# Kernel tuning notes

Hardware: AMD Instinct MI355X
Metric: run time of the kernel (lower is better)

The kernel has to match this reference:

```python
import jax, jax.numpy as jnp
import numpy as np

N = 1_000_000
H = 256
DIMS = [1, H, H, H, H]
N_LAYERS = 4  # 4 linear layers, sin activation after the first 3


def setup_inputs() -> dict:
    key = jax.random.key(0)
    ks = jax.random.split(key, 1 + 2 * N_LAYERS)
    d = {"x": jax.random.normal(ks[0], (N, 2), dtype=jnp.float32)}
    i = 1
    for pre in ("x", "t"):
        for l in range(N_LAYERS):
            lim = 1.0 / np.sqrt(DIMS[l])  # torch.nn.Linear default init range
            d[f"{pre}W{l}"] = jax.random.uniform(
                ks[i], (DIMS[l], DIMS[l + 1]), dtype=jnp.float32, minval=-lim, maxval=lim)
            d[f"{pre}b{l}"] = jnp.zeros((DIMS[l + 1],), dtype=jnp.float32)
            i += 1
    return d


def _mlp(h, params):
    # params: list of (W, b); sin activation after all but the last layer
    n = len(params)
    for idx, (W, b) in enumerate(params):
        h = h @ W + b
        if idx < n - 1:
            h = jnp.sin(h)
    return h


def reference(x, xW0, xb0, xW1, xb1, xW2, xb2, xW3, xb3,
              tW0, tb0, tW1, tb1, tW2, tb2, tW3, tb3):
    x_params = [(xW0, xb0), (xW1, xb1), (xW2, xb2), (xW3, xb3)]
    t_params = [(tW0, tb0), (tW1, tb1), (tW2, tb2), (tW3, tb3)]
    nx = _mlp(x[:, 0:1], x_params)  # [N, H]
    nt = _mlp(x[:, 1:2], t_params)  # [N, H]
    # diag(A @ B.T) == rowwise dot product; avoids the O(N^2) matmul
    even = jnp.sum(nx[:, 0::2] * nt[:, 0::2], axis=-1)  # [N]
    odd = jnp.sum(nx[:, 1::2] * nt[:, 1::2], axis=-1)   # [N]
    return jnp.stack([even, odd], axis=-1)  # [N, 2]
```

## Files before the change

### kernel.cpp

```cpp
#include <hip/hip_runtime.h>


typedef _Float16 f16x8 __attribute__((ext_vector_type(8)));
typedef _Float16 f16x4 __attribute__((ext_vector_type(4)));
typedef float f32x4 __attribute__((ext_vector_type(4)));

__device__ __forceinline__ int hswz(int m, int kbyte) {
    return m * 512 + ((((kbyte >> 4) ^ (m & 7)) & 31) << 4) + (kbyte & 15);
}

__device__ __forceinline__ void barrier_lds() {
    asm volatile("s_waitcnt lgkmcnt(0)" ::: "memory");
    __builtin_amdgcn_s_barrier();
}

__global__ void prepack(const float* __restrict__ xW1, const float* __restrict__ xW2,
                        const float* __restrict__ xW3, const float* __restrict__ tW1,
                        const float* __restrict__ tW2, const float* __restrict__ tW3,
                        _Float16* __restrict__ dst)
{
    int g = blockIdx.x * 256 + threadIdx.x;
    int L = g >> 16;
    int r = g & 65535;
    int j  = r & 7;
    int l  = (r >> 3) & 63;
    int ci = (r >> 9) & 1;
    int w  = (r >> 10) & 7;
    int gg = (r >> 13) & 7;
    const float* W;
    switch (L) {
        case 0: W = xW1; break;
        case 1: W = xW2; break;
        case 2: W = xW3; break;
        case 3: W = tW1; break;
        case 4: W = tW2; break;
        default: W = tW3; break;
    }
    int n = w * 32 + ci * 16 + (l & 15);
    int k = gg * 32 + ((l >> 4) & 3) * 8 + j;
    dst[g] = (_Float16)W[k * 256 + n];
}


__device__ __forceinline__ void layer0_scalar(
    float xv, const float* __restrict__ W0, const float* __restrict__ b0,
    _Float16* __restrict__ hb, int tid)
{
    int m = tid >> 2;
    int q = tid & 3;
#pragma unroll
    for (int g = 0; g < 8; ++g) {
        int n0 = g * 32 + q * 8;
        f16x8 hv;
#pragma unroll
        for (int e = 0; e < 8; ++e) {
            float z = fmaf(xv, W0[n0 + e], b0[n0 + e]);
            hv[e] = (_Float16)__sinf(z);
        }
        *(f16x8*)((char*)hb + hswz(m, n0 * 2)) = hv;
    }
}

template<int MODE>
__device__ __forceinline__ void gemm_phase(
    const _Float16* __restrict__ Wl,
    const _Float16* __restrict__ Wnext,
    const _Float16* __restrict__ rb,
    f32x4 acc[2][8], f16x8 afr[2][2],
    f32x4 wacc[2][8],
    const float* __restrict__ wbias,
    _Float16* __restrict__ wb_lds,
    float xv,
    const float* __restrict__ W0,
    const float* __restrict__ b0,
    int tid, int lane, int ln, int quad, int wave)
{
    f32x4 zero = {0.f, 0.f, 0.f, 0.f};
#pragma unroll
    for (int ci = 0; ci < 2; ++ci)
#pragma unroll
        for (int ri = 0; ri < 8; ++ri)
            acc[ci][ri] = zero;

    const _Float16* abase = Wl + wave * 1024 + lane * 8;

    f16x8 bfr[8];
#pragma unroll
    for (int ri = 0; ri < 8; ++ri)
        bfr[ri] = *(const f16x8*)((const char*)rb +
                                  hswz(16 * ri + ln, quad * 16));

#pragma unroll
    for (int g = 0; g < 8; ++g) {
        __builtin_amdgcn_s_setprio(1);
#pragma unroll
        for (int ci = 0; ci < 2; ++ci)
#pragma unroll
            for (int ri = 0; ri < 8; ++ri)
                acc[ci][ri] = __builtin_amdgcn_mfma_f32_16x16x32_f16(
                    afr[g & 1][ci], bfr[ri], acc[ci][ri], 0, 0, 0);
        __builtin_amdgcn_s_setprio(0);

        if (g < 7) {
#pragma unroll
            for (int ri = 0; ri < 8; ++ri)
                bfr[ri] = *(const f16x8*)((const char*)rb +
                              hswz(16 * ri + ln, (g + 1) * 64 + quad * 16));
        }
        if (g < 6) {
#pragma unroll
            for (int ci = 0; ci < 2; ++ci)
                afr[g & 1][ci] = *(const f16x8*)(abase + (g + 2) * 8192 + ci * 512);
        } else if (Wnext) {
#pragma unroll
            for (int ci = 0; ci < 2; ++ci)
                afr[g & 1][ci] = *(const f16x8*)(Wnext + (g - 6) * 8192 +
                                                 wave * 1024 + lane * 8 + ci * 512);
        }

        if (MODE == 1) {
#pragma unroll
            for (int jo = 0; jo < 2; ++jo) {
                const int s  = g * 2 + jo;
                const int cw = s >> 3, rw = s & 7;
                const int nb = wave * 32 + cw * 16 + quad * 4;
                f32x4 bv = *(const f32x4*)&wbias[nb];
                f16x4 hv;
                hv[0] = (_Float16)__sinf(wacc[cw][rw][0] + bv[0]);
                hv[1] = (_Float16)__sinf(wacc[cw][rw][1] + bv[1]);
                hv[2] = (_Float16)__sinf(wacc[cw][rw][2] + bv[2]);
                hv[3] = (_Float16)__sinf(wacc[cw][rw][3] + bv[3]);
                *(f16x4*)((char*)wb_lds + hswz(16 * rw + ln, nb * 2)) = hv;
            }
        } else if (MODE == 2) {
            const int m = tid >> 2, q = tid & 3;
            const int n0 = g * 32 + q * 8;
            f16x8 hv;
#pragma unroll
            for (int e = 0; e < 8; ++e) {
                float z = fmaf(xv, W0[n0 + e], b0[n0 + e]);
                hv[e] = (_Float16)__sinf(z);
            }
            *(f16x8*)((char*)wb_lds + hswz(m, n0 * 2)) = hv;
        }
    }
}

__global__ __launch_bounds__(512, 2)
void mlp_fused(const float* __restrict__ x,
               const float* __restrict__ xW0, const float* __restrict__ xb0,
               const float* __restrict__ xb1, const float* __restrict__ xb2,
               const float* __restrict__ xb3,
               const float* __restrict__ tW0, const float* __restrict__ tb0,
               const float* __restrict__ tb1, const float* __restrict__ tb2,
               const float* __restrict__ tb3,
               const _Float16* __restrict__ Wp,
               float* __restrict__ out, int N)
{
    __shared__ __align__(16) _Float16 hbuf[2][128 * 256];
    __shared__ __align__(16) float    params[10 * 256];

    const int tid = threadIdx.x;
    const int lane = tid & 63;
    const int wave = tid >> 6;
    const int ln = lane & 15;
    const int quad = lane >> 4;
    const int row0 = blockIdx.x * 128;

    {
        const float* psrc[10] = {xW0, xb0, tW0, tb0, xb1, xb2, xb3, tb1, tb2, tb3};
        int half = tid >> 8, e = tid & 255;
#pragma unroll
        for (int s = 0; s < 5; ++s)
            params[(half * 5 + s) * 256 + e] = psrc[half * 5 + s][e];
    }
    const int myrow = row0 + (tid >> 2);
    const float2 xv2 = (myrow < N) ? ((const float2*)x)[myrow]
                                   : make_float2(0.f, 0.f);

    f32x4 xacc[2][8], tacc[2][8];
    f16x8 afr[2][2];

#pragma unroll
    for (int s = 0; s < 2; ++s)
#pragma unroll
        for (int ci = 0; ci < 2; ++ci)
            afr[s][ci] = *(const f16x8*)(Wp + s * 8192 + wave * 1024 +
                                         lane * 8 + ci * 512);
    barrier_lds();

    layer0_scalar(xv2.x, &params[0], &params[256], hbuf[0], tid);
    barrier_lds();

    gemm_phase<2>(Wp + 0 * 65536, Wp + 3 * 65536, hbuf[0], xacc, afr,
                  nullptr, nullptr, hbuf[1],
                  xv2.y, &params[2 * 256], &params[3 * 256],
                  tid, lane, ln, quad, wave);
    barrier_lds();
    gemm_phase<1>(Wp + 3 * 65536, Wp + 1 * 65536, hbuf[1], tacc, afr,
                  xacc, &params[4 * 256], hbuf[0],
                  0.f, nullptr, nullptr, tid, lane, ln, quad, wave);
    barrier_lds();
    gemm_phase<1>(Wp + 1 * 65536, Wp + 4 * 65536, hbuf[0], xacc, afr,
                  tacc, &params[7 * 256], hbuf[1],
                  0.f, nullptr, nullptr, tid, lane, ln, quad, wave);
    barrier_lds();
    gemm_phase<1>(Wp + 4 * 65536, Wp + 2 * 65536, hbuf[1], tacc, afr,
                  xacc, &params[5 * 256], hbuf[0],
                  0.f, nullptr, nullptr, tid, lane, ln, quad, wave);
    barrier_lds();
    gemm_phase<1>(Wp + 2 * 65536, Wp + 5 * 65536, hbuf[0], xacc, afr,
                  tacc, &params[8 * 256], hbuf[1],
                  0.f, nullptr, nullptr, tid, lane, ln, quad, wave);
    barrier_lds();
    gemm_phase<0>(Wp + 5 * 65536, nullptr, hbuf[1], tacc, afr,
                  nullptr, nullptr, nullptr,
                  0.f, nullptr, nullptr, tid, lane, ln, quad, wave);

    const float* xb3l = &params[6 * 256];
    const float* tb3l = &params[9 * 256];
    float ev[8], od[8];
#pragma unroll
    for (int ri = 0; ri < 8; ++ri) { ev[ri] = 0.f; od[ri] = 0.f; }
#pragma unroll
    for (int ci = 0; ci < 2; ++ci) {
        int nb = wave * 32 + ci * 16 + quad * 4;
        f32x4 xb = *(const f32x4*)&xb3l[nb];
        f32x4 tb = *(const f32x4*)&tb3l[nb];
#pragma unroll
        for (int ri = 0; ri < 8; ++ri) {
            float a0 = xacc[ci][ri][0] + xb[0], c0 = tacc[ci][ri][0] + tb[0];
            float a1 = xacc[ci][ri][1] + xb[1], c1 = tacc[ci][ri][1] + tb[1];
            float a2 = xacc[ci][ri][2] + xb[2], c2 = tacc[ci][ri][2] + tb[2];
            float a3 = xacc[ci][ri][3] + xb[3], c3 = tacc[ci][ri][3] + tb[3];
            ev[ri] += a0 * c0 + a2 * c2;
            od[ri] += a1 * c1 + a3 * c3;
        }
    }
#pragma unroll
    for (int ri = 0; ri < 8; ++ri) {
        ev[ri] += __shfl_xor(ev[ri], 16, 64);
        ev[ri] += __shfl_xor(ev[ri], 32, 64);
        od[ri] += __shfl_xor(od[ri], 16, 64);
        od[ri] += __shfl_xor(od[ri], 32, 64);
    }

    float* red = (float*)hbuf[0];
    if (lane < 16) {
#pragma unroll
        for (int ri = 0; ri < 8; ++ri) {
            red[wave * 256 + ri * 32 + ln * 2 + 0] = ev[ri];
            red[wave * 256 + ri * 32 + ln * 2 + 1] = od[ri];
        }
    }
    __syncthreads();
    if (tid < 256) {
        int p = tid & 1, row = tid >> 1;
        int base = (row >> 4) * 32 + (row & 15) * 2 + p;
        float s = 0.f;
#pragma unroll
        for (int w = 0; w < 8; ++w)
            s += red[w * 256 + base];
        if (row0 + row < N)
            out[(row0 + row) * 2 + p] = s;
    }
}

extern "C" void kernel_launch(void* const* d_in, const int* in_sizes, int n_in,
                              void* d_out, int out_size, void* d_ws, size_t ws_size,
                              hipStream_t stream)
{
    const float* x   = (const float*)d_in[0];
    const float* xW0 = (const float*)d_in[1];
    const float* xb0 = (const float*)d_in[2];
    const float* xW1 = (const float*)d_in[3];
    const float* xb1 = (const float*)d_in[4];
    const float* xW2 = (const float*)d_in[5];
    const float* xb2 = (const float*)d_in[6];
    const float* xW3 = (const float*)d_in[7];
    const float* xb3 = (const float*)d_in[8];
    const float* tW0 = (const float*)d_in[9];
    const float* tb0 = (const float*)d_in[10];
    const float* tW1 = (const float*)d_in[11];
    const float* tb1 = (const float*)d_in[12];
    const float* tW2 = (const float*)d_in[13];
    const float* tb2 = (const float*)d_in[14];
    const float* tW3 = (const float*)d_in[15];
    const float* tb3 = (const float*)d_in[16];

    _Float16* Wp = (_Float16*)d_ws;
    const int N = in_sizes[0] / 2;
    const int nblk = (N + 127) / 128;

    prepack<<<1536, 256, 0, stream>>>(xW1, xW2, xW3, tW1, tW2, tW3, Wp);
    mlp_fused<<<nblk, 512, 0, stream>>>(x, xW0, xb0, xb1, xb2, xb3,
                                        tW0, tb0, tb1, tb2, tb3,
                                        Wp, (float*)d_out, N);
}
```

Baseline: 865.0 us.

## Stagger per-wave K order and split B-fragment loads into half-tile double buffer

Each wave now walks the K dimension starting at its own offset (g0 = wave), so waves read different LDS regions and weight chunks at the same moment and LDS bank and broadcast contention drops. B fragments are loaded in two halves of four, and the second half's load overlaps the first half's MFMAs. The sin/bias writeback is interleaved between the two MFMA halves. This cuts register pressure for B fragments, at the cost of more load instructions and rotating index arithmetic. K-order rotation changes the fp32 summation order slightly.

```diff
diff --git a/kernel.cpp b/kernel.cpp
--- a/kernel.cpp
+++ b/kernel.cpp
@@ -73,7 +73,7 @@
     float xv,
     const float* __restrict__ W0,
     const float* __restrict__ b0,
-    int tid, int lane, int ln, int quad, int wave)
+    int tid, int lane, int ln, int quad, int wave, int g0)
 {
     f32x4 zero = {0.f, 0.f, 0.f, 0.f};
 #pragma unroll
@@ -84,57 +84,85 @@
 
     const _Float16* abase = Wl + wave * 1024 + lane * 8;
 
-    f16x8 bfr[8];
-#pragma unroll
-    for (int ri = 0; ri < 8; ++ri)
-        bfr[ri] = *(const f16x8*)((const char*)rb +
-                                  hswz(16 * ri + ln, quad * 16));
-
-#pragma unroll
-    for (int g = 0; g < 8; ++g) {
+    f16x8 bfr[2][4];
+#pragma unroll
+    for (int r = 0; r < 4; ++r)
+        bfr[0][r] = *(const f16x8*)((const char*)rb +
+                                    hswz(16 * r + ln, g0 * 64 + quad * 16));
+
+#pragma unroll
+    for (int t = 0; t < 8; ++t) {
+        const int gs  = (g0 + t) & 7;
+        const int gs1 = (g0 + t + 1) & 7;
+
+#pragma unroll
+        for (int r = 0; r < 4; ++r)
+            bfr[1][r] = *(const f16x8*)((const char*)rb +
+                            hswz(16 * (r + 4) + ln, gs * 64 + quad * 16));
+
         __builtin_amdgcn_s_setprio(1);
 #pragma unroll
         for (int ci = 0; ci < 2; ++ci)
 #pragma unroll
-            for (int ri = 0; ri < 8; ++ri)
-                acc[ci][ri] = __builtin_amdgcn_mfma_f32_16x16x32_f16(
-                    afr[g & 1][ci], bfr[ri], acc[ci][ri], 0, 0, 0);
+            for (int r = 0; r < 4; ++r)
+                acc[ci][r] = __builtin_amdgcn_mfma_f32_16x16x32_f16(
+                    afr[t & 1][ci], bfr[0][r], acc[ci][r], 0, 0, 0);
         __builtin_amdgcn_s_setprio(0);
 
-        if (g < 7) {
-#pragma unroll
-            for (int ri = 0; ri < 8; ++ri)
-                bfr[ri] = *(const f16x8*)((const char*)rb +
-                              hswz(16 * ri + ln, (g + 1) * 64 + quad * 16));
-        }
-        if (g < 6) {
+        if (MODE == 1) {
+            const int s = 2 * t, cw = s >> 3, rw = s & 7;
+            const int nb = wave * 32 + cw * 16 + quad * 4;
+            f32x4 bv = *(const f32x4*)&wbias[nb];
+            f16x4 hv;
+            hv[0] = (_Float16)__sinf(wacc[cw][rw][0] + bv[0]);
+            hv[1] = (_Float16)__sinf(wacc[cw][rw][1] + bv[1]);
+            hv[2] = (_Float16)__sinf(wacc[cw][rw][2] + bv[2]);
+            hv[3] = (_Float16)__sinf(wacc[cw][rw][3] + bv[3]);
+            *(f16x4*)((char*)wb_lds + hswz(16 * rw + ln, nb * 2)) = hv;
+        }
+
+        if (t < 7) {
+#pragma unroll
+            for (int r = 0; r < 4; ++r)
+                bfr[0][r] = *(const f16x8*)((const char*)rb +
+                                hswz(16 * r + ln, gs1 * 64 + quad * 16));
+        }
+
+        __builtin_amdgcn_s_setprio(1);
+#pragma unroll
+        for (int ci = 0; ci < 2; ++ci)
+#pragma unroll
+            for (int r = 0; r < 4; ++r)
+                acc[ci][r + 4] = __builtin_amdgcn_mfma_f32_16x16x32_f16(
+                    afr[t & 1][ci], bfr[1][r], acc[ci][r + 4], 0, 0, 0);
+        __builtin_amdgcn_s_setprio(0);
+
+        if (t < 6) {
+            const int gs2 = (g0 + t + 2) & 7;
 #pragma unroll
             for (int ci = 0; ci < 2; ++ci)
-                afr[g & 1][ci] = *(const f16x8*)(abase + (g + 2) * 8192 + ci * 512);
+                afr[t & 1][ci] = *(const f16x8*)(abase + gs2 * 8192 + ci * 512);
         } else if (Wnext) {
+            const int gs2 = (g0 + t + 2) & 7;
 #pragma unroll
             for (int ci = 0; ci < 2; ++ci)
-                afr[g & 1][ci] = *(const f16x8*)(Wnext + (g - 6) * 8192 +
+                afr[t & 1][ci] = *(const f16x8*)(Wnext + gs2 * 8192 +
                                                  wave * 1024 + lane * 8 + ci * 512);
         }
 
         if (MODE == 1) {
-#pragma unroll
-            for (int jo = 0; jo < 2; ++jo) {
-                const int s  = g * 2 + jo;
-                const int cw = s >> 3, rw = s & 7;
-                const int nb = wave * 32 + cw * 16 + quad * 4;
-                f32x4 bv = *(const f32x4*)&wbias[nb];
-                f16x4 hv;
-                hv[0] = (_Float16)__sinf(wacc[cw][rw][0] + bv[0]);
-                hv[1] = (_Float16)__sinf(wacc[cw][rw][1] + bv[1]);
-                hv[2] = (_Float16)__sinf(wacc[cw][rw][2] + bv[2]);
-                hv[3] = (_Float16)__sinf(wacc[cw][rw][3] + bv[3]);
-                *(f16x4*)((char*)wb_lds + hswz(16 * rw + ln, nb * 2)) = hv;
-            }
+            const int s = 2 * t + 1, cw = s >> 3, rw = s & 7;
+            const int nb = wave * 32 + cw * 16 + quad * 4;
+            f32x4 bv = *(const f32x4*)&wbias[nb];
+            f16x4 hv;
+            hv[0] = (_Float16)__sinf(wacc[cw][rw][0] + bv[0]);
+            hv[1] = (_Float16)__sinf(wacc[cw][rw][1] + bv[1]);
+            hv[2] = (_Float16)__sinf(wacc[cw][rw][2] + bv[2]);
+            hv[3] = (_Float16)__sinf(wacc[cw][rw][3] + bv[3]);
+            *(f16x4*)((char*)wb_lds + hswz(16 * rw + ln, nb * 2)) = hv;
         } else if (MODE == 2) {
             const int m = tid >> 2, q = tid & 3;
-            const int n0 = g * 32 + q * 8;
+            const int n0 = t * 32 + q * 8;
             f16x8 hv;
 #pragma unroll
             for (int e = 0; e < 8; ++e) {
@@ -166,6 +194,7 @@
     const int ln = lane & 15;
     const int quad = lane >> 4;
     const int row0 = blockIdx.x * 128;
+    const int g0 = wave;
 
     {
         const float* psrc[10] = {xW0, xb0, tW0, tb0, xb1, xb2, xb3, tb1, tb2, tb3};
@@ -182,11 +211,13 @@
     f16x8 afr[2][2];
 
 #pragma unroll
-    for (int s = 0; s < 2; ++s)
+    for (int s = 0; s < 2; ++s) {
+        const int gs = (g0 + s) & 7;
 #pragma unroll
         for (int ci = 0; ci < 2; ++ci)
-            afr[s][ci] = *(const f16x8*)(Wp + s * 8192 + wave * 1024 +
+            afr[s][ci] = *(const f16x8*)(Wp + gs * 8192 + wave * 1024 +
                                          lane * 8 + ci * 512);
+    }
     barrier_lds();
 
     layer0_scalar(xv2.x, &params[0], &params[256], hbuf[0], tid);
@@ -195,27 +226,27 @@
     gemm_phase<2>(Wp + 0 * 65536, Wp + 3 * 65536, hbuf[0], xacc, afr,
                   nullptr, nullptr, hbuf[1],
                   xv2.y, &params[2 * 256], &params[3 * 256],
-                  tid, lane, ln, quad, wave);
+                  tid, lane, ln, quad, wave, g0);
     barrier_lds();
     gemm_phase<1>(Wp + 3 * 65536, Wp + 1 * 65536, hbuf[1], tacc, afr,
                   xacc, &params[4 * 256], hbuf[0],
-                  0.f, nullptr, nullptr, tid, lane, ln, quad, wave);
+                  0.f, nullptr, nullptr, tid, lane, ln, quad, wave, g0);
     barrier_lds();
     gemm_phase<1>(Wp + 1 * 65536, Wp + 4 * 65536, hbuf[0], xacc, afr,
                   tacc, &params[7 * 256], hbuf[1],
-                  0.f, nullptr, nullptr, tid, lane, ln, quad, wave);
+                  0.f, nullptr, nullptr, tid, lane, ln, quad, wave, g0);
     barrier_lds();
     gemm_phase<1>(Wp + 4 * 65536, Wp + 2 * 65536, hbuf[1], tacc, afr,
                   xacc, &params[5 * 256], hbuf[0],
-                  0.f, nullptr, nullptr, tid, lane, ln, quad, wave);
+                  0.f, nullptr, nullptr, tid, lane, ln, quad, wave, g0);
     barrier_lds();
     gemm_phase<1>(Wp + 2 * 65536, Wp + 5 * 65536, hbuf[0], xacc, afr,
                   tacc, &params[8 * 256], hbuf[1],
-                  0.f, nullptr, nullptr, tid, lane, ln, quad, wave);
+                  0.f, nullptr, nullptr, tid, lane, ln, quad, wave, g0);
     barrier_lds();
     gemm_phase<0>(Wp + 5 * 65536, nullptr, hbuf[1], tacc, afr,
                   nullptr, nullptr, nullptr,
-                  0.f, nullptr, nullptr, tid, lane, ln, quad, wave);
+                  0.f, nullptr, nullptr, tid, lane, ln, quad, wave, g0);
 
     const float* xb3l = &params[6 * 256];
     const float* tb3l = &params[9 * 256];
```

Result: slower. 1.148 ms (+32.7%).

## Split B-fragment loads into two halves and interleave epilogue sin with MFMAs

Applied to the files above, without the earlier changes.

The per-step MFMA block is split into two halves of four row tiles, with the second-half B fragments loaded before the first MFMA group and the first-half fragments for the next step loaded between groups. The previous layer's sin/bias epilogue writes are spread between the two MFMA groups so LDS reads and stores can overlap matrix work. The launch bound is relaxed from 2 to 1 blocks per SM, giving the compiler more registers but possibly lowering occupancy. Parameter loading into LDS now uses only 256 threads.

```diff
diff --git a/kernel.cpp b/kernel.cpp
--- a/kernel.cpp
+++ b/kernel.cpp
@@ -84,29 +84,56 @@
 
     const _Float16* abase = Wl + wave * 1024 + lane * 8;
 
-    f16x8 bfr[8];
-#pragma unroll
-    for (int ri = 0; ri < 8; ++ri)
-        bfr[ri] = *(const f16x8*)((const char*)rb +
-                                  hswz(16 * ri + ln, quad * 16));
+    f16x8 bfr[2][4];
+#pragma unroll
+    for (int r = 0; r < 4; ++r)
+        bfr[0][r] = *(const f16x8*)((const char*)rb +
+                                    hswz(16 * r + ln, quad * 16));
 
 #pragma unroll
     for (int g = 0; g < 8; ++g) {
+#pragma unroll
+        for (int r = 0; r < 4; ++r)
+            bfr[1][r] = *(const f16x8*)((const char*)rb +
+                            hswz(16 * (r + 4) + ln, g * 64 + quad * 16));
+
         __builtin_amdgcn_s_setprio(1);
 #pragma unroll
         for (int ci = 0; ci < 2; ++ci)
 #pragma unroll
-            for (int ri = 0; ri < 8; ++ri)
-                acc[ci][ri] = __builtin_amdgcn_mfma_f32_16x16x32_f16(
-                    afr[g & 1][ci], bfr[ri], acc[ci][ri], 0, 0, 0);
+            for (int r = 0; r < 4; ++r)
+                acc[ci][r] = __builtin_amdgcn_mfma_f32_16x16x32_f16(
+                    afr[g & 1][ci], bfr[0][r], acc[ci][r], 0, 0, 0);
         __builtin_amdgcn_s_setprio(0);
 
+        if (MODE == 1) {
+            const int s = 2 * g, cw = s >> 3, rw = s & 7;
+            const int nb = wave * 32 + cw * 16 + quad * 4;
+            f32x4 bv = *(const f32x4*)&wbias[nb];
+            f16x4 hv;
+            hv[0] = (_Float16)__sinf(wacc[cw][rw][0] + bv[0]);
+            hv[1] = (_Float16)__sinf(wacc[cw][rw][1] + bv[1]);
+            hv[2] = (_Float16)__sinf(wacc[cw][rw][2] + bv[2]);
+            hv[3] = (_Float16)__sinf(wacc[cw][rw][3] + bv[3]);
+            *(f16x4*)((char*)wb_lds + hswz(16 * rw + ln, nb * 2)) = hv;
+        }
+
         if (g < 7) {
 #pragma unroll
-            for (int ri = 0; ri < 8; ++ri)
-                bfr[ri] = *(const f16x8*)((const char*)rb +
-                              hswz(16 * ri + ln, (g + 1) * 64 + quad * 16));
-        }
+            for (int r = 0; r < 4; ++r)
+                bfr[0][r] = *(const f16x8*)((const char*)rb +
+                                hswz(16 * r + ln, (g + 1) * 64 + quad * 16));
+        }
+
+        __builtin_amdgcn_s_setprio(1);
+#pragma unroll
+        for (int ci = 0; ci < 2; ++ci)
+#pragma unroll
+            for (int r = 0; r < 4; ++r)
+                acc[ci][r + 4] = __builtin_amdgcn_mfma_f32_16x16x32_f16(
+                    afr[g & 1][ci], bfr[1][r], acc[ci][r + 4], 0, 0, 0);
+        __builtin_amdgcn_s_setprio(0);
+
         if (g < 6) {
 #pragma unroll
             for (int ci = 0; ci < 2; ++ci)
@@ -119,19 +146,15 @@
         }
 
         if (MODE == 1) {
-#pragma unroll
-            for (int jo = 0; jo < 2; ++jo) {
-                const int s  = g * 2 + jo;
-                const int cw = s >> 3, rw = s & 7;
-                const int nb = wave * 32 + cw * 16 + quad * 4;
-                f32x4 bv = *(const f32x4*)&wbias[nb];
-                f16x4 hv;
-                hv[0] = (_Float16)__sinf(wacc[cw][rw][0] + bv[0]);
-                hv[1] = (_Float16)__sinf(wacc[cw][rw][1] + bv[1]);
-                hv[2] = (_Float16)__sinf(wacc[cw][rw][2] + bv[2]);
-                hv[3] = (_Float16)__sinf(wacc[cw][rw][3] + bv[3]);
-                *(f16x4*)((char*)wb_lds + hswz(16 * rw + ln, nb * 2)) = hv;
-            }
+            const int s = 2 * g + 1, cw = s >> 3, rw = s & 7;
+            const int nb = wave * 32 + cw * 16 + quad * 4;
+            f32x4 bv = *(const f32x4*)&wbias[nb];
+            f16x4 hv;
+            hv[0] = (_Float16)__sinf(wacc[cw][rw][0] + bv[0]);
+            hv[1] = (_Float16)__sinf(wacc[cw][rw][1] + bv[1]);
+            hv[2] = (_Float16)__sinf(wacc[cw][rw][2] + bv[2]);
+            hv[3] = (_Float16)__sinf(wacc[cw][rw][3] + bv[3]);
+            *(f16x4*)((char*)wb_lds + hswz(16 * rw + ln, nb * 2)) = hv;
         } else if (MODE == 2) {
             const int m = tid >> 2, q = tid & 3;
             const int n0 = g * 32 + q * 8;
@@ -146,7 +169,7 @@
     }
 }
 
-__global__ __launch_bounds__(512, 2)
+__global__ __launch_bounds__(512, 1)
 void mlp_fused(const float* __restrict__ x,
                const float* __restrict__ xW0, const float* __restrict__ xb0,
                const float* __restrict__ xb1, const float* __restrict__ xb2,
@@ -167,12 +190,11 @@
     const int quad = lane >> 4;
     const int row0 = blockIdx.x * 128;
 
-    {
+    if (tid < 256) {
         const float* psrc[10] = {xW0, xb0, tW0, tb0, xb1, xb2, xb3, tb1, tb2, tb3};
-        int half = tid >> 8, e = tid & 255;
-#pragma unroll
-        for (int s = 0; s < 5; ++s)
-            params[(half * 5 + s) * 256 + e] = psrc[half * 5 + s][e];
+#pragma unroll
+        for (int s = 0; s < 10; ++s)
+            params[s * 256 + tid] = psrc[s][tid];
     }
     const int myrow = row0 + (tid >> 2);
     const float2 xv2 = (myrow < N) ? ((const float2*)x)[myrow]
```

Result: no change. 851.6 us (-1.6%).
